# Kernel tuning notes

Hardware: AMD Instinct MI355X
Metric: run time of the kernel (lower is better)

The kernel has to match this reference:

```python
import jax, jax.numpy as jnp
import numpy as np

N_NODES = 50000
N_EDGES = 600000
N_GRAPHS = 64
D_FEAT = 128
DIM_H = 128
N_HOPS = 3
OUT_DIM = 10


def setup_inputs() -> dict:
    key = jax.random.key(0)
    ks = jax.random.split(key, 16)
    x = jax.random.normal(ks[0], (N_NODES, D_FEAT), dtype=jnp.float32)
    edge_index = jax.random.randint(ks[1], (2, N_EDGES), 0, N_NODES, dtype=jnp.int64)
    batch = jnp.sort(jax.random.randint(ks[2], (N_NODES,), 0, N_GRAPHS, dtype=jnp.int64))
    def glorot(k, shape):
        fan = shape[0] + shape[1]
        return jax.random.uniform(k, shape, jnp.float32, -1.0, 1.0) * np.sqrt(6.0 / fan)
    # GCNConv weights stored as [in, out]; Linear weights stored as [in, out]
    W1 = glorot(ks[3], (D_FEAT, DIM_H)); b1 = jnp.zeros((DIM_H,), jnp.float32)
    W2 = glorot(ks[4], (DIM_H, DIM_H)); b2 = jnp.zeros((DIM_H,), jnp.float32)
    W3 = glorot(ks[5], (DIM_H, DIM_H)); b3 = jnp.zeros((DIM_H,), jnp.float32)
    H3 = DIM_H * N_HOPS
    lin1_W = glorot(ks[6], (H3, H3)); lin1_b = jnp.zeros((H3,), jnp.float32)
    lin2_W = glorot(ks[7], (H3, OUT_DIM)); lin2_b = jnp.zeros((OUT_DIM,), jnp.float32)
    return {"x": x, "W1": W1, "b1": b1, "W2": W2, "b2": b2, "W3": W3, "b3": b3,
            "lin1_W": lin1_W, "lin1_b": lin1_b, "lin2_W": lin2_W, "lin2_b": lin2_b,
            "edge_index": edge_index, "batch": batch}


def gcn_conv(x, W, b, src, dst, n_nodes):
    # PyG GCNConv (add_self_loops=True, normalize=True):
    #   deg[i] = in-degree at target + 1 (self loop); norm = d^-1/2[src] * d^-1/2[dst]
    deg = jnp.zeros((n_nodes,), x.dtype).at[dst].add(1.0) + 1.0
    dinv = jax.lax.rsqrt(deg)
    xw = x @ W  # [N, H] transform before propagate
    coef = (dinv[src] * dinv[dst])[:, None]
    agg = jnp.zeros_like(xw).at[dst].add(xw[src] * coef)
    agg = agg + xw * (dinv * dinv)[:, None]  # self-loop messages
    return agg + b


def global_mean_pool(h, batch, n_graphs):
    sums = jax.ops.segment_sum(h, batch, num_segments=n_graphs)
    cnt = jax.ops.segment_sum(jnp.ones((h.shape[0],), h.dtype), batch, num_segments=n_graphs)
    return sums / jnp.maximum(cnt, 1.0)[:, None]


def reference(x, W1, b1, W2, b2, W3, b3, lin1_W, lin1_b, lin2_W, lin2_b, edge_index, batch):
    src, dst = edge_index[0], edge_index[1]
    n = x.shape[0]
    h1 = gcn_conv(x, W1, b1, src, dst, n)
    h2 = gcn_conv(h1, W2, b2, src, dst, n)
    h3 = gcn_conv(h2, W3, b3, src, dst, n)
    pooled = jnp.concatenate([global_mean_pool(h, batch, N_GRAPHS) for h in (h1, h2, h3)], axis=1)
    h = jax.nn.relu(pooled @ lin1_W + lin1_b)
    # dropout is identity in eval mode
    h = h @ lin2_W + lin2_b
    return (h, jax.nn.log_softmax(h, axis=1))
```

## Files before the change

### kernel.cpp

```cpp
#include <hip/hip_runtime.h>
#include <hip/hip_fp16.h>
#include <math.h>

#define N_NODES 50000
#define N_EDGES 600000
#define N_GRAPHS 64
#define DFEAT 128
#define H3 384
#define OUTD 10
#define SCAN_BLOCKS 196
#define POOL_CHUNKS 16
#define APAD 136

typedef _Float16 f16x8 __attribute__((ext_vector_type(8)));
typedef float f32x4 __attribute__((ext_vector_type(4)));

__global__ __launch_bounds__(256) void k_deg(const int* __restrict__ ei, int* __restrict__ deg) {
    int e = blockIdx.x * 256 + threadIdx.x;
    if (e >= N_EDGES) return;
    int dst = ei[N_EDGES + e];
    atomicAdd(&deg[dst], 1);
}

__global__ __launch_bounds__(256) void k_part(const int* __restrict__ deg, int* __restrict__ part) {
    __shared__ int red[256];
    int tid = threadIdx.x;
    int i = blockIdx.x * 256 + tid;
    red[tid] = (i < N_NODES) ? deg[i] : 0;
    __syncthreads();
    for (int s = 128; s > 0; s >>= 1) {
        if (tid < s) red[tid] += red[tid + s];
        __syncthreads();
    }
    if (tid == 0) part[blockIdx.x] = red[0];
}

__global__ __launch_bounds__(256) void k_scanpart(const int* __restrict__ part, int* __restrict__ base) {
    __shared__ int buf[256];
    int tid = threadIdx.x;
    int v = (tid < SCAN_BLOCKS) ? part[tid] : 0;
    buf[tid] = v;
    __syncthreads();
    for (int d = 1; d < 256; d <<= 1) {
        int t = (tid >= d) ? buf[tid - d] : 0;
        __syncthreads();
        buf[tid] += t;
        __syncthreads();
    }
    if (tid < SCAN_BLOCKS) base[tid] = buf[tid] - v;
}

__global__ __launch_bounds__(256) void k_offsets(const int* __restrict__ deg, const int* __restrict__ base,
                                                 int* __restrict__ offs, int* __restrict__ cursor,
                                                 float* __restrict__ dinv) {
    __shared__ int buf[256];
    int tid = threadIdx.x;
    int i = blockIdx.x * 256 + tid;
    int v = (i < N_NODES) ? deg[i] : 0;
    buf[tid] = v;
    __syncthreads();
    for (int d = 1; d < 256; d <<= 1) {
        int t = (tid >= d) ? buf[tid - d] : 0;
        __syncthreads();
        buf[tid] += t;
        __syncthreads();
    }
    if (i < N_NODES) {
        int excl = base[blockIdx.x] + buf[tid] - v;
        offs[i] = excl;
        cursor[i] = excl;
        dinv[i] = rsqrtf((float)v + 1.0f);
        if (i == N_NODES - 1) offs[N_NODES] = base[blockIdx.x] + buf[tid];
    }
}

__global__ __launch_bounds__(256) void k_fill(const int* __restrict__ ei, int* __restrict__ cursor,
                                              int* __restrict__ srcs) {
    int e = blockIdx.x * 256 + threadIdx.x;
    if (e >= N_EDGES) return;
    int s = ei[e];
    int t = ei[N_EDGES + e];
    int pos = atomicAdd(&cursor[t], 1);
    srcs[pos] = s;
}

__global__ __launch_bounds__(256) void k_prep(const float* __restrict__ W1, const float* __restrict__ W2,
                                              const float* __restrict__ W3, _Float16* __restrict__ Wt,
                                              float* __restrict__ pooled) {
    int b = blockIdx.x;
    if (b < 192) {
        int idx = b * 256 + threadIdx.x;
        int l = idx >> 14, r = idx & 16383;
        const float* W = (l == 0) ? W1 : (l == 1) ? W2 : W3;
        int k = r >> 7, n = r & 127;
        Wt[l * 16384 + n * 128 + k] = (_Float16)W[k * 128 + n];
    } else {
        int idx = (b - 192) * 256 + threadIdx.x;
        if (idx < N_GRAPHS * H3) pooled[idx] = 0.0f;
    }
}

template <bool A_FP16>
__global__ __launch_bounds__(256) void gemm_mfma(const void* __restrict__ Aptr, const _Float16* __restrict__ Wt,
                                                 __half* __restrict__ T, int M) {
    __shared__ _Float16 As[64 * APAD];
    __shared__ _Float16 Ws[128 * APAD];
    int tid = threadIdx.x;
    int base = blockIdx.x * 64;
    for (int c = tid; c < 2048; c += 256) {
        int n = c >> 4, c8 = (c & 15) << 3;
        *(f16x8*)&Ws[n * APAD + c8] = *(const f16x8*)&Wt[n * 128 + c8];
    }
    for (int c = tid; c < 1024; c += 256) {
        int r = c >> 4, c8 = (c & 15) << 3;
        int gr = base + r; if (gr >= M) gr = M - 1;
        if (A_FP16) {
            const _Float16* A = (const _Float16*)Aptr;
            *(f16x8*)&As[r * APAD + c8] = *(const f16x8*)&A[(size_t)gr * 128 + c8];
        } else {
            const float* A = (const float*)Aptr;
            const float* src = A + (size_t)gr * 128 + c8;
            float4 v0 = *(const float4*)(src);
            float4 v1 = *(const float4*)(src + 4);
            f16x8 h;
            h[0] = (_Float16)v0.x; h[1] = (_Float16)v0.y; h[2] = (_Float16)v0.z; h[3] = (_Float16)v0.w;
            h[4] = (_Float16)v1.x; h[5] = (_Float16)v1.y; h[6] = (_Float16)v1.z; h[7] = (_Float16)v1.w;
            *(f16x8*)&As[r * APAD + c8] = h;
        }
    }
    __syncthreads();
    int wave = tid >> 6, lane = tid & 63;
    int m = lane & 15, quad = lane >> 4;
    f32x4 acc[8];
#pragma unroll
    for (int ct = 0; ct < 8; ++ct) acc[ct] = (f32x4){0.f, 0.f, 0.f, 0.f};
#pragma unroll
    for (int kc = 0; kc < 4; ++kc) {
        f16x8 a = *(const f16x8*)&As[(wave * 16 + m) * APAD + kc * 32 + quad * 8];
#pragma unroll
        for (int ct = 0; ct < 8; ++ct) {
            f16x8 b = *(const f16x8*)&Ws[(ct * 16 + m) * APAD + kc * 32 + quad * 8];
            acc[ct] = __builtin_amdgcn_mfma_f32_16x16x32_f16(b, a, acc[ct], 0, 0, 0);
        }
    }
    int node = base + wave * 16 + m;
    if (node < M) {
#pragma unroll
        for (int ct = 0; ct < 8; ++ct) {
            int col = ct * 16 + quad * 4;
            __half2 h0 = __floats2half2_rn(acc[ct][0], acc[ct][1]);
            __half2 h1 = __floats2half2_rn(acc[ct][2], acc[ct][3]);
            *(__half2*)(T + (size_t)node * 128 + col)     = h0;
            *(__half2*)(T + (size_t)node * 128 + col + 2) = h1;
        }
    }
}

__global__ __launch_bounds__(128) void gather_agg(const __half2* __restrict__ T2, const int* __restrict__ srcs,
                                                  const int* __restrict__ offs,
                                                  const float* __restrict__ dinv, const float* __restrict__ bias,
                                                  __half2* __restrict__ H2) {
    int node = blockIdx.x * 2 + (threadIdx.x >> 6);
    int lane = threadIdx.x & 63;
    if (node >= N_NODES) return;
    float di = dinv[node];
    float2 b2 = *(const float2*)(bias + lane * 2);
    float2 sf = __half22float2(T2[(size_t)node * 64 + lane]);
    float sx = 0.0f, sy = 0.0f;
    int lo = offs[node], hi = offs[node + 1];
    int e = lo;
    for (; e + 8 <= hi; e += 8) {
        int s0 = srcs[e + 0], s1 = srcs[e + 1], s2 = srcs[e + 2], s3 = srcs[e + 3];
        int s4 = srcs[e + 4], s5 = srcs[e + 5], s6 = srcs[e + 6], s7 = srcs[e + 7];
        float c0 = dinv[s0], c1 = dinv[s1], c2 = dinv[s2], c3 = dinv[s3];
        float c4 = dinv[s4], c5 = dinv[s5], c6 = dinv[s6], c7 = dinv[s7];
        float2 t0 = __half22float2(T2[(size_t)s0 * 64 + lane]);
        float2 t1 = __half22float2(T2[(size_t)s1 * 64 + lane]);
        float2 t2 = __half22float2(T2[(size_t)s2 * 64 + lane]);
        float2 t3 = __half22float2(T2[(size_t)s3 * 64 + lane]);
        float2 t4 = __half22float2(T2[(size_t)s4 * 64 + lane]);
        float2 t5 = __half22float2(T2[(size_t)s5 * 64 + lane]);
        float2 t6 = __half22float2(T2[(size_t)s6 * 64 + lane]);
        float2 t7 = __half22float2(T2[(size_t)s7 * 64 + lane]);
        sx += t0.x * c0; sy += t0.y * c0;
        sx += t1.x * c1; sy += t1.y * c1;
        sx += t2.x * c2; sy += t2.y * c2;
        sx += t3.x * c3; sy += t3.y * c3;
        sx += t4.x * c4; sy += t4.y * c4;
        sx += t5.x * c5; sy += t5.y * c5;
        sx += t6.x * c6; sy += t6.y * c6;
        sx += t7.x * c7; sy += t7.y * c7;
    }
    for (; e + 4 <= hi; e += 4) {
        int s0 = srcs[e + 0], s1 = srcs[e + 1], s2 = srcs[e + 2], s3 = srcs[e + 3];
        float c0 = dinv[s0], c1 = dinv[s1], c2 = dinv[s2], c3 = dinv[s3];
        float2 t0 = __half22float2(T2[(size_t)s0 * 64 + lane]);
        float2 t1 = __half22float2(T2[(size_t)s1 * 64 + lane]);
        float2 t2 = __half22float2(T2[(size_t)s2 * 64 + lane]);
        float2 t3 = __half22float2(T2[(size_t)s3 * 64 + lane]);
        sx += t0.x * c0; sy += t0.y * c0;
        sx += t1.x * c1; sy += t1.y * c1;
        sx += t2.x * c2; sy += t2.y * c2;
        sx += t3.x * c3; sy += t3.y * c3;
    }
    for (; e < hi; ++e) {
        int s = srcs[e];
        float c = dinv[s];
        float2 t = __half22float2(T2[(size_t)s * 64 + lane]);
        sx += t.x * c; sy += t.y * c;
    }
    float accx = di * sx + sf.x * (di * di) + b2.x;
    float accy = di * sy + sf.y * (di * di) + b2.y;
    H2[(size_t)node * 64 + lane] = __floats2half2_rn(accx, accy);
}

__global__ __launch_bounds__(256) void pool_kernel(const __half2* __restrict__ H2, const int* __restrict__ batch,
                                                   float* __restrict__ pooled, float* __restrict__ cnt,
                                                   int colOff) {
    __shared__ int bounds[2];
    __shared__ float2 red[256];
    int g = blockIdx.x >> 4;
    int chunk = blockIdx.x & (POOL_CHUNKS - 1);
    int tid = threadIdx.x;
    int d2 = tid & 63, sub = tid >> 6;
    if (tid < 2) {
        int target = g + tid;
        int lo = 0, hi = N_NODES;
        while (lo < hi) {
            int mid = (lo + hi) >> 1;
            if (batch[mid] < target) lo = mid + 1; else hi = mid;
        }
        bounds[tid] = lo;
    }
    __syncthreads();
    int lo = bounds[0], hi = bounds[1];
    int n = hi - lo;
    int per = (n + POOL_CHUNKS - 1) / POOL_CHUNKS;
    int s = lo + chunk * per;
    int e = s + per; if (e > hi) e = hi;
    float ax = 0.0f, ay = 0.0f;
    for (int r = s + sub; r < e; r += 4) {
        float2 v = __half22float2(H2[(size_t)r * 64 + d2]);
        ax += v.x; ay += v.y;
    }
    red[tid] = make_float2(ax, ay);
    __syncthreads();
    if (sub == 0 && s < e) {
        float2 v0 = red[d2], v1 = red[64 + d2], v2 = red[128 + d2], v3 = red[192 + d2];
        float vx = v0.x + v1.x + v2.x + v3.x;
        float vy = v0.y + v1.y + v2.y + v3.y;
        atomicAdd(&pooled[g * H3 + colOff + d2 * 2],     vx);
        atomicAdd(&pooled[g * H3 + colOff + d2 * 2 + 1], vy);
    }
    if (chunk == 0 && tid == 0) cnt[g] = (float)n;
}

__global__ __launch_bounds__(384) void mlp_kernel(const float* __restrict__ pooled,
                                                  const float* __restrict__ cnt,
                                                  const float* __restrict__ l1W, const float* __restrict__ l1b,
                                                  const float* __restrict__ l2W, const float* __restrict__ l2b,
                                                  float* __restrict__ out) {
    __shared__ float p[H3];
    __shared__ float hid[H3];
    __shared__ float o10[OUTD];
    int g = blockIdx.x, tid = threadIdx.x;
    float inv = 1.0f / fmaxf(cnt[g], 1.0f);
    p[tid] = pooled[g * H3 + tid] * inv;
    __syncthreads();
    float acc = l1b[tid];
    for (int k = 0; k < H3; ++k) acc += p[k] * l1W[k * H3 + tid];
    hid[tid] = fmaxf(acc, 0.0f);
    __syncthreads();
    if (tid < OUTD) {
        float o = l2b[tid];
        for (int k = 0; k < H3; ++k) o += hid[k] * l2W[k * OUTD + tid];
        o10[tid] = o;
        out[g * OUTD + tid] = o;
    }
    __syncthreads();
    if (tid == 0) {
        float m = o10[0];
        for (int j = 1; j < OUTD; ++j) m = fmaxf(m, o10[j]);
        float s = 0.0f;
        for (int j = 0; j < OUTD; ++j) s += expf(o10[j] - m);
        float lse = m + logf(s);
        for (int j = 0; j < OUTD; ++j) out[N_GRAPHS * OUTD + g * OUTD + j] = o10[j] - lse;
    }
}

extern "C" void kernel_launch(void* const* d_in, const int* in_sizes, int n_in,
                              void* d_out, int out_size, void* d_ws, size_t ws_size,
                              hipStream_t stream) {
    const float* x      = (const float*)d_in[0];
    const float* W1     = (const float*)d_in[1];
    const float* b1     = (const float*)d_in[2];
    const float* W2     = (const float*)d_in[3];
    const float* b2     = (const float*)d_in[4];
    const float* W3     = (const float*)d_in[5];
    const float* b3     = (const float*)d_in[6];
    const float* lin1_W = (const float*)d_in[7];
    const float* lin1_b = (const float*)d_in[8];
    const float* lin2_W = (const float*)d_in[9];
    const float* lin2_b = (const float*)d_in[10];
    const int* edge_index = (const int*)d_in[11];
    const int* batch      = (const int*)d_in[12];

    char* ws = (char*)d_ws;
    auto alloc = [&](size_t bytes) -> void* {
        void* p = (void*)ws;
        ws += (bytes + 255) & ~(size_t)255;
        return p;
    };
    int*   deg    = (int*)  alloc((size_t)N_NODES * 4);
    int*   part   = (int*)  alloc((size_t)SCAN_BLOCKS * 4);
    int*   pbase  = (int*)  alloc((size_t)SCAN_BLOCKS * 4);
    int*   offs   = (int*)  alloc((size_t)(N_NODES + 1) * 4);
    int*   cursor = (int*)  alloc((size_t)N_NODES * 4);
    float* dinv   = (float*)alloc((size_t)N_NODES * 4);
    int*   srcs   = (int*)  alloc((size_t)N_EDGES * 4);
    __half* T     = (__half*)alloc((size_t)N_NODES * 128 * 2);
    __half* H     = (__half*)alloc((size_t)N_NODES * 128 * 2);
    _Float16* Wt  = (_Float16*)alloc((size_t)3 * 128 * 128 * 2);
    float* pooled = (float*)alloc((size_t)N_GRAPHS * H3 * 4);
    float* cnt    = (float*)alloc((size_t)N_GRAPHS * 4);

    hipMemsetAsync(deg, 0, (size_t)N_NODES * 4, stream);
    k_deg<<<(N_EDGES + 255) / 256, 256, 0, stream>>>(edge_index, deg);
    k_part<<<SCAN_BLOCKS, 256, 0, stream>>>(deg, part);
    k_scanpart<<<1, 256, 0, stream>>>(part, pbase);
    k_offsets<<<SCAN_BLOCKS, 256, 0, stream>>>(deg, pbase, offs, cursor, dinv);
    k_fill<<<(N_EDGES + 255) / 256, 256, 0, stream>>>(edge_index, cursor, srcs);
    k_prep<<<288, 256, 0, stream>>>(W1, W2, W3, Wt, pooled);

    const float* bs[3] = {b1, b2, b3};
    for (int l = 0; l < 3; ++l) {
        if (l == 0)
            gemm_mfma<false><<<(N_NODES + 63) / 64, 256, 0, stream>>>(x, Wt, T, N_NODES);
        else
            gemm_mfma<true><<<(N_NODES + 63) / 64, 256, 0, stream>>>(H, Wt + (size_t)l * 16384, T, N_NODES);
        gather_agg<<<(N_NODES + 1) / 2, 128, 0, stream>>>((const __half2*)T, srcs, offs, dinv, bs[l], (__half2*)H);
        pool_kernel<<<N_GRAPHS * POOL_CHUNKS, 256, 0, stream>>>((const __half2*)H, batch, pooled, cnt, l * 128);
    }
    mlp_kernel<<<N_GRAPHS, 384, 0, stream>>>(pooled, cnt, lin1_W, lin1_b, lin2_W, lin2_b, (float*)d_out);
}
```

Measured before the change: 337.0 us.

## Fuse mean-pool into gather aggregation and precompute CSR fill ranks

```diff
diff --git a/kernel.cpp b/kernel.cpp
--- a/kernel.cpp
+++ b/kernel.cpp
@@ -9,17 +9,17 @@
 #define H3 384
 #define OUTD 10
 #define SCAN_BLOCKS 196
-#define POOL_CHUNKS 16
 #define APAD 136
 
 typedef _Float16 f16x8 __attribute__((ext_vector_type(8)));
 typedef float f32x4 __attribute__((ext_vector_type(4)));
 
-__global__ __launch_bounds__(256) void k_deg(const int* __restrict__ ei, int* __restrict__ deg) {
+__global__ __launch_bounds__(256) void k_deg(const int* __restrict__ ei, int* __restrict__ deg,
+                                             int* __restrict__ rank) {
     int e = blockIdx.x * 256 + threadIdx.x;
     if (e >= N_EDGES) return;
     int dst = ei[N_EDGES + e];
-    atomicAdd(&deg[dst], 1);
+    rank[e] = atomicAdd(&deg[dst], 1);
 }
 
 __global__ __launch_bounds__(256) void k_part(const int* __restrict__ deg, int* __restrict__ part) {
@@ -51,8 +51,7 @@
 }
 
 __global__ __launch_bounds__(256) void k_offsets(const int* __restrict__ deg, const int* __restrict__ base,
-                                                 int* __restrict__ offs, int* __restrict__ cursor,
-                                                 float* __restrict__ dinv) {
+                                                 int* __restrict__ offs, float* __restrict__ dinv) {
     __shared__ int buf[256];
     int tid = threadIdx.x;
     int i = blockIdx.x * 256 + tid;
@@ -68,20 +67,18 @@
     if (i < N_NODES) {
         int excl = base[blockIdx.x] + buf[tid] - v;
         offs[i] = excl;
-        cursor[i] = excl;
         dinv[i] = rsqrtf((float)v + 1.0f);
         if (i == N_NODES - 1) offs[N_NODES] = base[blockIdx.x] + buf[tid];
     }
 }
 
-__global__ __launch_bounds__(256) void k_fill(const int* __restrict__ ei, int* __restrict__ cursor,
-                                              int* __restrict__ srcs) {
+__global__ __launch_bounds__(256) void k_fill(const int* __restrict__ ei, const int* __restrict__ offs,
+                                              const int* __restrict__ rank, int* __restrict__ srcs) {
     int e = blockIdx.x * 256 + threadIdx.x;
     if (e >= N_EDGES) return;
     int s = ei[e];
     int t = ei[N_EDGES + e];
-    int pos = atomicAdd(&cursor[t], 1);
-    srcs[pos] = s;
+    srcs[offs[t] + rank[e]] = s;
 }
 
 __global__ __launch_bounds__(256) void k_prep(const float* __restrict__ W1, const float* __restrict__ W2,
@@ -156,13 +153,16 @@
     }
 }
 
-__global__ __launch_bounds__(128) void gather_agg(const __half2* __restrict__ T2, const int* __restrict__ srcs,
-                                                  const int* __restrict__ offs,
-                                                  const float* __restrict__ dinv, const float* __restrict__ bias,
-                                                  __half2* __restrict__ H2) {
-    int node = blockIdx.x * 2 + (threadIdx.x >> 6);
-    int lane = threadIdx.x & 63;
-    if (node >= N_NODES) return;
+__global__ __launch_bounds__(512) void gather_pool(const __half2* __restrict__ T2, const int* __restrict__ srcs,
+                                                   const int* __restrict__ offs,
+                                                   const float* __restrict__ dinv, const float* __restrict__ bias,
+                                                   const int* __restrict__ batch,
+                                                   __half2* __restrict__ H2, float* __restrict__ pooled,
+                                                   int colOff, int storeH) {
+    __shared__ float2 psum[8][64];
+    __shared__ int pg[8];
+    int wave = threadIdx.x >> 6, lane = threadIdx.x & 63;
+    int node = blockIdx.x * 8 + wave;
     float di = dinv[node];
     float2 b2 = *(const float2*)(bias + lane * 2);
     float2 sf = __half22float2(T2[(size_t)node * 64 + lane]);
@@ -211,18 +211,41 @@
     }
     float accx = di * sx + sf.x * (di * di) + b2.x;
     float accy = di * sy + sf.y * (di * di) + b2.y;
-    H2[(size_t)node * 64 + lane] = __floats2half2_rn(accx, accy);
-}
-
-__global__ __launch_bounds__(256) void pool_kernel(const __half2* __restrict__ H2, const int* __restrict__ batch,
-                                                   float* __restrict__ pooled, float* __restrict__ cnt,
-                                                   int colOff) {
-    __shared__ int bounds[2];
-    __shared__ float2 red[256];
-    int g = blockIdx.x >> 4;
-    int chunk = blockIdx.x & (POOL_CHUNKS - 1);
-    int tid = threadIdx.x;
-    int d2 = tid & 63, sub = tid >> 6;
+    if (storeH) H2[(size_t)node * 64 + lane] = __floats2half2_rn(accx, accy);
+    psum[wave][lane] = make_float2(accx, accy);
+    if (lane == 0) pg[wave] = batch[node];
+    __syncthreads();
+    if (wave == 0) {
+        int g0 = pg[0];
+        bool uni = (pg[1] == g0) & (pg[2] == g0) & (pg[3] == g0) &
+                   (pg[4] == g0) & (pg[5] == g0) & (pg[6] == g0) & (pg[7] == g0);
+        if (uni) {
+            float vx = 0.0f, vy = 0.0f;
+#pragma unroll
+            for (int w = 0; w < 8; ++w) { float2 v = psum[w][lane]; vx += v.x; vy += v.y; }
+            atomicAdd(&pooled[g0 * H3 + colOff + lane * 2],     vx);
+            atomicAdd(&pooled[g0 * H3 + colOff + lane * 2 + 1], vy);
+        } else {
+#pragma unroll
+            for (int w = 0; w < 8; ++w) {
+                float2 v = psum[w][lane];
+                atomicAdd(&pooled[pg[w] * H3 + colOff + lane * 2],     v.x);
+                atomicAdd(&pooled[pg[w] * H3 + colOff + lane * 2 + 1], v.y);
+            }
+        }
+    }
+}
+
+__global__ __launch_bounds__(384) void mlp_kernel(const float* __restrict__ pooled,
+                                                  const int* __restrict__ batch,
+                                                  const float* __restrict__ l1W, const float* __restrict__ l1b,
+                                                  const float* __restrict__ l2W, const float* __restrict__ l2b,
+                                                  float* __restrict__ out) {
+    __shared__ float p[H3];
+    __shared__ float hid[H3];
+    __shared__ float o10[OUTD];
+    __shared__ int bnd[2];
+    int g = blockIdx.x, tid = threadIdx.x;
     if (tid < 2) {
         int target = g + tid;
         int lo = 0, hi = N_NODES;
@@ -230,41 +253,10 @@
             int mid = (lo + hi) >> 1;
             if (batch[mid] < target) lo = mid + 1; else hi = mid;
         }
-        bounds[tid] = lo;
-    }
-    __syncthreads();
-    int lo = bounds[0], hi = bounds[1];
-    int n = hi - lo;
-    int per = (n + POOL_CHUNKS - 1) / POOL_CHUNKS;
-    int s = lo + chunk * per;
-    int e = s + per; if (e > hi) e = hi;
-    float ax = 0.0f, ay = 0.0f;
-    for (int r = s + sub; r < e; r += 4) {
-        float2 v = __half22float2(H2[(size_t)r * 64 + d2]);
-        ax += v.x; ay += v.y;
-    }
-    red[tid] = make_float2(ax, ay);
-    __syncthreads();
-    if (sub == 0 && s < e) {
-        float2 v0 = red[d2], v1 = red[64 + d2], v2 = red[128 + d2], v3 = red[192 + d2];
-        float vx = v0.x + v1.x + v2.x + v3.x;
-        float vy = v0.y + v1.y + v2.y + v3.y;
-        atomicAdd(&pooled[g * H3 + colOff + d2 * 2],     vx);
-        atomicAdd(&pooled[g * H3 + colOff + d2 * 2 + 1], vy);
-    }
-    if (chunk == 0 && tid == 0) cnt[g] = (float)n;
-}
-
-__global__ __launch_bounds__(384) void mlp_kernel(const float* __restrict__ pooled,
-                                                  const float* __restrict__ cnt,
-                                                  const float* __restrict__ l1W, const float* __restrict__ l1b,
-                                                  const float* __restrict__ l2W, const float* __restrict__ l2b,
-                                                  float* __restrict__ out) {
-    __shared__ float p[H3];
-    __shared__ float hid[H3];
-    __shared__ float o10[OUTD];
-    int g = blockIdx.x, tid = threadIdx.x;
-    float inv = 1.0f / fmaxf(cnt[g], 1.0f);
+        bnd[tid] = lo;
+    }
+    __syncthreads();
+    float inv = 1.0f / fmaxf((float)(bnd[1] - bnd[0]), 1.0f);
     p[tid] = pooled[g * H3 + tid] * inv;
     __syncthreads();
     float acc = l1b[tid];
@@ -315,21 +307,20 @@
     int*   part   = (int*)  alloc((size_t)SCAN_BLOCKS * 4);
     int*   pbase  = (int*)  alloc((size_t)SCAN_BLOCKS * 4);
     int*   offs   = (int*)  alloc((size_t)(N_NODES + 1) * 4);
-    int*   cursor = (int*)  alloc((size_t)N_NODES * 4);
+    int*   rank   = (int*)  alloc((size_t)N_EDGES * 4);
     float* dinv   = (float*)alloc((size_t)N_NODES * 4);
     int*   srcs   = (int*)  alloc((size_t)N_EDGES * 4);
     __half* T     = (__half*)alloc((size_t)N_NODES * 128 * 2);
     __half* H     = (__half*)alloc((size_t)N_NODES * 128 * 2);
     _Float16* Wt  = (_Float16*)alloc((size_t)3 * 128 * 128 * 2);
     float* pooled = (float*)alloc((size_t)N_GRAPHS * H3 * 4);
-    float* cnt    = (float*)alloc((size_t)N_GRAPHS * 4);
 
     hipMemsetAsync(deg, 0, (size_t)N_NODES * 4, stream);
-    k_deg<<<(N_EDGES + 255) / 256, 256, 0, stream>>>(edge_index, deg);
+    k_deg<<<(N_EDGES + 255) / 256, 256, 0, stream>>>(edge_index, deg, rank);
     k_part<<<SCAN_BLOCKS, 256, 0, stream>>>(deg, part);
     k_scanpart<<<1, 256, 0, stream>>>(part, pbase);
-    k_offsets<<<SCAN_BLOCKS, 256, 0, stream>>>(deg, pbase, offs, cursor, dinv);
-    k_fill<<<(N_EDGES + 255) / 256, 256, 0, stream>>>(edge_index, cursor, srcs);
+    k_offsets<<<SCAN_BLOCKS, 256, 0, stream>>>(deg, pbase, offs, dinv);
+    k_fill<<<(N_EDGES + 255) / 256, 256, 0, stream>>>(edge_index, offs, rank, srcs);
     k_prep<<<288, 256, 0, stream>>>(W1, W2, W3, Wt, pooled);
 
     const float* bs[3] = {b1, b2, b3};
@@ -338,8 +329,8 @@
             gemm_mfma<false><<<(N_NODES + 63) / 64, 256, 0, stream>>>(x, Wt, T, N_NODES);
         else
             gemm_mfma<true><<<(N_NODES + 63) / 64, 256, 0, stream>>>(H, Wt + (size_t)l * 16384, T, N_NODES);
-        gather_agg<<<(N_NODES + 1) / 2, 128, 0, stream>>>((const __half2*)T, srcs, offs, dinv, bs[l], (__half2*)H);
-        pool_kernel<<<N_GRAPHS * POOL_CHUNKS, 256, 0, stream>>>((const __half2*)H, batch, pooled, cnt, l * 128);
-    }
-    mlp_kernel<<<N_GRAPHS, 384, 0, stream>>>(pooled, cnt, lin1_W, lin1_b, lin2_W, lin2_b, (float*)d_out);
-}
+        gather_pool<<<N_NODES / 8, 512, 0, stream>>>((const __half2*)T, srcs, offs, dinv, bs[l], batch,
+                                                     (__half2*)H, pooled, l * 128, (l < 2) ? 1 : 0);
+    }
+    mlp_kernel<<<N_GRAPHS, 384, 0, stream>>>(pooled, batch, lin1_W, lin1_b, lin2_W, lin2_b, (float*)d_out);
+}
```

New measurement: 350.8 us. +4.1%, slower.
